# Kernel tuning notes

Measured on AMD Instinct MI355X. Metric: run time of the kernel, lower is better.

The kernel has to match this reference:

```python
import jax, jax.numpy as jnp
import numpy as np

B, L, D = 2, 4096, 1024      # batch, seq_len, d_model (expand_ratio=1 -> d_inner == D)
DS, RK, K = 16, 64, 3        # d_state, dt_rank, conv kernel size
EPS = 1e-5


def setup_inputs() -> dict:
    key = jax.random.key(0)
    ks = jax.random.split(key, 16)
    s = 0.02
    inp = {
        "x":      jax.random.normal(ks[0], (B, L, D), jnp.float32),
        "gamma":  jnp.ones((D,), jnp.float32),
        "beta":   jnp.zeros((D,), jnp.float32),
        "W_in":   jax.random.normal(ks[1], (D, 2 * D), jnp.float32) * s,
        "conv_w": jax.random.normal(ks[2], (K, 1, D), jnp.float32) * s,   # depthwise (k, 1, d)
        "conv_b": jnp.zeros((D,), jnp.float32),
        "W_xp":   jax.random.normal(ks[3], (D, RK), jnp.float32) * s,
        "W_Bg":   jax.random.normal(ks[4], (D, DS), jnp.float32) * s,
        "W_Cg":   jax.random.normal(ks[5], (D, DS), jnp.float32) * s,
        "W_dt":   jax.random.normal(ks[6], (RK, D), jnp.float32) * s,
        "b_dt":   jnp.zeros((D,), jnp.float32),
        "W_Bp":   jax.random.normal(ks[7], (DS, D), jnp.float32) * s,
        "W_Cp":   jax.random.normal(ks[8], (DS, D), jnp.float32) * s,
        "A":      -jnp.exp(jax.random.normal(ks[9], (D,), jnp.float32) * 0.5),  # negative for stability
        "D_skip": jnp.ones((D,), jnp.float32),
        "W_out":  jax.random.normal(ks[10], (D, D), jnp.float32) * s,
    }
    return inp


def reference(x, gamma, beta, W_in, conv_w, conv_b, W_xp, W_Bg, W_Cg,
              W_dt, b_dt, W_Bp, W_Cp, A, D_skip, W_out):
    d = x.shape[-1]
    # 1. LayerNorm
    mu = jnp.mean(x, -1, keepdims=True)
    var = jnp.mean(jnp.square(x - mu), -1, keepdims=True)
    xn = (x - mu) * jax.lax.rsqrt(var + EPS) * gamma + beta
    # 2. in_proj + split into main/gate branch
    xz = xn @ W_in                                 # (b, l, 2d)
    xb, z = jnp.split(xz, 2, axis=-1)
    # 3. depthwise Conv1D (same padding) + SiLU
    xc = jax.lax.conv_general_dilated(
        xb, conv_w, window_strides=(1,), padding='SAME',
        dimension_numbers=('NWC', 'WIO', 'NWC'), feature_group_count=d) + conv_b
    x_act = jax.nn.silu(xc)                        # (b, l, d)
    # SSM parameter generation
    delta = jax.nn.softplus((x_act @ W_xp) @ W_dt + b_dt)   # (b, l, d)
    Bm = (x_act @ W_Bg) @ W_Bp                     # (b, l, d)
    Cm = (x_act @ W_Cg) @ W_Cp                     # (b, l, d)
    # 4. diagonal selective scan: h_t = exp(delta*A)*h_{t-1} + delta*B*x ; y = C*h
    dA = jnp.exp(delta * A)
    dBx = delta * Bm * x_act
    def step(h, ab):
        a, bx = ab
        h = a * h + bx
        return h, h
    h0 = jnp.zeros_like(dA[:, 0])
    _, hs = jax.lax.scan(step, h0, (dA.transpose(1, 0, 2), dBx.transpose(1, 0, 2)))
    y = Cm * hs.transpose(1, 0, 2)
    # 5. skip-D, gating, out_proj + residual
    out_ssm = y + x_act * D_skip
    gated = out_ssm * jax.nn.silu(z)
    return gated @ W_out + x
```

## Files before the change

kernel.cpp:

```cpp
#include <hip/hip_runtime.h>
#include <math.h>

#define BB 2
#define LL 4096
#define DD 1024
#define DS 16
#define RK 64
#define MM (BB*LL)
#define NC 128
#define LC (LL/NC)

typedef __attribute__((ext_vector_type(8))) short short8;
typedef __attribute__((ext_vector_type(4))) float f32x4;

__device__ __forceinline__ unsigned short f2bf(float f) {
    union { float f; unsigned u; } v; v.f = f;
    unsigned r = v.u + 0x7fff + ((v.u >> 16) & 1);
    return (unsigned short)(r >> 16);
}
__device__ __forceinline__ float bf2f(unsigned short u) {
    union { unsigned u; float f; } v; v.u = ((unsigned)u) << 16;
    return v.f;
}
__device__ __forceinline__ float2 bf2x2(unsigned u) {
    return make_float2(bf2f((unsigned short)u), bf2f((unsigned short)(u >> 16)));
}
__device__ __forceinline__ unsigned f2bfx2(float lo, float hi) {
    return (unsigned)f2bf(lo) | ((unsigned)f2bf(hi) << 16);
}
__device__ __forceinline__ float fast_rcp(float x) {
    return __builtin_amdgcn_rcpf(x);
}
__device__ __forceinline__ float silu_f(float v) {
    return v * fast_rcp(1.0f + __expf(-v));
}
__device__ __forceinline__ void gload16(const void* g, void* l) {
    __builtin_amdgcn_global_load_lds(
        (const __attribute__((address_space(1))) unsigned int*)g,
        (__attribute__((address_space(3))) unsigned int*)l, 16, 0, 0);
}

__global__ __launch_bounds__(256)
void prep_misc(const float* __restrict__ W_in, const float* __restrict__ W_out,
               const float* __restrict__ W_xp, const float* __restrict__ W_Bg,
               const float* __restrict__ W_Cg, const float* __restrict__ W_dt,
               const float* __restrict__ W_Bp, const float* __restrict__ W_Cp,
               unsigned short* __restrict__ WinT, unsigned short* __restrict__ WoutT,
               unsigned short* __restrict__ WgT, unsigned short* __restrict__ WdtT,
               float* __restrict__ WBpT, float* __restrict__ WCpT,
               const float* __restrict__ x, const float* __restrict__ gamma,
               const float* __restrict__ beta, unsigned short* __restrict__ xn_bf) {
    __shared__ float t[32][33];
    __shared__ float ss[4], qq[4];
    int b = blockIdx.x;
    if (b >= 4224) {
        int row = b - 4224;
        int tid = threadIdx.x;
        const float4* xr = (const float4*)(x + (size_t)row * DD);
        float4 v = xr[tid];
        float s = v.x + v.y + v.z + v.w;
        float q = v.x*v.x + v.y*v.y + v.z*v.z + v.w*v.w;
        #pragma unroll
        for (int off = 32; off > 0; off >>= 1) {
            s += __shfl_down(s, off);
            q += __shfl_down(q, off);
        }
        int wv = tid >> 6;
        if ((tid & 63) == 0) { ss[wv] = s; qq[wv] = q; }
        __syncthreads();
        float S = ss[0] + ss[1] + ss[2] + ss[3];
        float Q = qq[0] + qq[1] + qq[2] + qq[3];
        float mu  = S * (1.0f / DD);
        float var = Q * (1.0f / DD) - mu * mu;
        float r = rsqrtf(var + 1e-5f);
        int d0 = tid * 4;
        float4 gv = *(const float4*)(gamma + d0);
        float4 bv = *(const float4*)(beta + d0);
        ushort4 o;
        o.x = f2bf((v.x - mu) * r * gv.x + bv.x);
        o.y = f2bf((v.y - mu) * r * gv.y + bv.y);
        o.z = f2bf((v.z - mu) * r * gv.z + bv.z);
        o.w = f2bf((v.w - mu) * r * gv.w + bv.w);
        *(ushort4*)&xn_bf[(size_t)row * DD + d0] = o;
    } else if (b < 3072) {
        const float* W; unsigned short* WT; int K, N, n0, k0;
        if (b < 2048) { W = W_in;  WT = WinT;  K = DD; N = 2 * DD;
                        n0 = (b & 63) * 32; k0 = (b >> 6) * 32; }
        else { int bb = b - 2048; W = W_out; WT = WoutT; K = DD; N = DD;
               n0 = (bb & 31) * 32; k0 = (bb >> 5) * 32; }
        int tx = threadIdx.x & 31, ty = threadIdx.x >> 5;
        #pragma unroll
        for (int r = 0; r < 32; r += 8)
            t[ty + r][tx] = W[(size_t)(k0 + ty + r) * N + n0 + tx];
        __syncthreads();
        #pragma unroll
        for (int r = 0; r < 32; r += 8) {
            int nl = ty + r;
            WT[(size_t)(n0 + nl) * K + k0 + tx] = f2bf(t[tx][nl]);
        }
    } else if (b < 3584) {
        int idx = (b - 3072) * 256 + threadIdx.x;
        int k = idx & 1023, n = idx >> 10;
        float v = 0.0f;
        if (n < 64)       v = W_xp[k * RK + n];
        else if (n < 80)  v = W_Bg[k * DS + (n - 64)];
        else if (n < 96)  v = W_Cg[k * DS + (n - 80)];
        WgT[idx] = f2bf(v);
    } else if (b < 4096) {
        int idx = (b - 3584) * 256 + threadIdx.x;
        int k = idx & 127, n = idx >> 7;
        float v = (k < 64) ? W_dt[k * 1024 + n] : 0.0f;
        WdtT[idx] = f2bf(v);
    } else if (b < 4160) {
        int idx = (b - 4096) * 256 + threadIdx.x;
        WBpT[idx] = W_Bp[(idx & 15) * 1024 + (idx >> 4)];
    } else {
        int idx = (b - 4160) * 256 + threadIdx.x;
        WCpT[idx] = W_Cp[(idx & 15) * 1024 + (idx >> 4)];
    }
}

#define MF(a, b, c) __builtin_amdgcn_mfma_f32_16x16x32_bf16(a, b, c, 0, 0, 0)
template<int EPI, int BM>
__global__ __launch_bounds__(512, 1)
void gemm256(const unsigned short* __restrict__ A, const unsigned short* __restrict__ BT,
             void* __restrict__ C0v, void* __restrict__ C1v,
             const float* __restrict__ res, int M, int N, int K) {
    constexpr int MR = BM / 32;
    constexpr int RA = BM / 64;
    constexpr int ABUF = BM * 64;
    extern __shared__ unsigned short sm[];
    unsigned short* As = sm;
    unsigned short* Bs = sm + 2 * ABUF;
    const int tid = threadIdx.x;
    const int wave = tid >> 6, lane = tid & 63;
    const int wr = wave >> 2, wc = wave & 3;
    const int fr = lane & 15, fs = lane >> 4;

    int nbx = gridDim.x;
    int nwg = nbx * gridDim.y;
    int bid = blockIdx.y * nbx + blockIdx.x;
    int cpx = nwg >> 3;
    int swz = (bid & 7) * cpx + (bid >> 3);
    int by = swz / nbx, bx = swz - by * nbx;
    size_t rb = (size_t)by * BM, cb = (size_t)bx * 256;

    const int srow = tid >> 3;
    const int ssw  = (tid & 7) ^ (srow & 7);
    const unsigned short* gA = A + (rb + srow) * K + ssw * 8;
    const unsigned short* gB = BT + (cb + srow) * K + ssw * 8;
    const size_t rstep = (size_t)64 * K;
    unsigned short* dA = As + tid * 8;
    unsigned short* dB = Bs + tid * 8;
    const int T = K >> 6;

#define STGA(rnd, buf, kt) gload16(gA + (size_t)(rnd) * rstep + (size_t)(kt) * 64, dA + (buf) * ABUF + (rnd) * 4096)
#define STGB(rnd, buf, kt) gload16(gB + (size_t)(rnd) * rstep + (size_t)(kt) * 64, dB + (buf) * 16384 + (rnd) * 4096)
#define FOFF(r, S) (((r) << 6) + ((((S) ^ ((r) & 7))) << 3))
#define LDA(i, kk) (*(const short8*)&Ab[FOFF(arow0 + ((i) << 4), fs + ((kk) << 2))])
#define LDB(j, kk) (*(const short8*)&Bb[FOFF(brow0 + ((j) << 4), fs + ((kk) << 2))])

    const int arow0 = wr * (BM / 2) + fr;
    const int brow0 = wc * 64 + fr;

    f32x4 acc[MR][4] = {};

    #pragma unroll
    for (int r = 0; r < RA; ++r) STGA(r, 0, 0);
    #pragma unroll
    for (int r = 0; r < 4; ++r) STGB(r, 0, 0);

    #pragma unroll 1
    for (int t = 0; t < T; ++t) {
        const int cur = t & 1, nx = cur ^ 1;
        const bool pf = (t + 1) < T;
        const unsigned short* Ab = As + cur * ABUF;
        const unsigned short* Bb = Bs + cur * 16384;

        if (pf) { STGA(0, nx, t + 1); STGB(0, nx, t + 1); }
        if (pf) { asm volatile("s_waitcnt vmcnt(2)" ::: "memory"); }
        else    { asm volatile("s_waitcnt vmcnt(0)" ::: "memory"); }
        __builtin_amdgcn_s_barrier();
        __builtin_amdgcn_sched_barrier(0);

        short8 bfr[4][2];
        #pragma unroll
        for (int j = 0; j < 4; ++j) {
            bfr[j][0] = LDB(j, 0);
            bfr[j][1] = LDB(j, 1);
        }
        __builtin_amdgcn_s_setprio(1);
        #pragma unroll
        for (int ii = 0; ii < MR / 4; ++ii) {
            short8 a0 = LDA(ii, 0), a1 = LDA(ii, 1);
            #pragma unroll
            for (int j = 0; j < 4; ++j) {
                acc[ii][j] = MF(a0, bfr[j][0], acc[ii][j]);
                acc[ii][j] = MF(a1, bfr[j][1], acc[ii][j]);
            }
        }
        __builtin_amdgcn_s_setprio(0);
        __builtin_amdgcn_sched_barrier(0);

        #pragma unroll
        for (int p = 1; p < 4; ++p) {
            if (pf) {
                if (p < RA) STGA(p, nx, t + 1);
                STGB(p, nx, t + 1);
            }
            __builtin_amdgcn_s_setprio(1);
            #pragma unroll
            for (int ii = 0; ii < MR / 4; ++ii) {
                const int i = p * (MR / 4) + ii;
                short8 a0 = LDA(i, 0), a1 = LDA(i, 1);
                #pragma unroll
                for (int j = 0; j < 4; ++j) {
                    acc[i][j] = MF(a0, bfr[j][0], acc[i][j]);
                    acc[i][j] = MF(a1, bfr[j][1], acc[i][j]);
                }
            }
            __builtin_amdgcn_s_setprio(0);
            __builtin_amdgcn_sched_barrier(0);
        }
        __builtin_amdgcn_s_barrier();
    }

    const int row0 = (int)rb + wr * (BM / 2) + fs * 4;
    const int col0 = (int)cb + wc * 64 + fr;
    if (EPI == 1) {
        unsigned short* Cd = (cb < DD) ? (unsigned short*)C0v : (unsigned short*)C1v;
        const int cadj = (cb < DD) ? 0 : -DD;
        #pragma unroll
        for (int i = 0; i < MR; ++i)
            #pragma unroll
            for (int j = 0; j < 4; ++j) {
                int col = col0 + cadj + (j << 4);
                #pragma unroll
                for (int q = 0; q < 4; ++q)
                    Cd[(size_t)(row0 + (i << 4) + q) * DD + col] = f2bf(acc[i][j][q]);
            }
    } else {
        float* C0 = (float*)C0v;
        #pragma unroll
        for (int i = 0; i < MR; ++i)
            #pragma unroll
            for (int j = 0; j < 4; ++j) {
                int col = col0 + (j << 4);
                #pragma unroll
                for (int q = 0; q < 4; ++q) {
                    size_t off = (size_t)(row0 + (i << 4) + q) * N + col;
                    C0[off] = acc[i][j][q] + res[off];
                }
            }
    }
#undef STGA
#undef STGB
#undef FOFF
#undef LDA
#undef LDB
}

__global__ __launch_bounds__(256)
void gemm_up(const unsigned short* __restrict__ A, const unsigned short* __restrict__ BT,
             unsigned short* __restrict__ C, const float* __restrict__ bias, int N) {
    __shared__ unsigned short As[128 * 128];
    __shared__ unsigned short Bs[128 * 128];
    int tid = threadIdx.x;
    int rb = blockIdx.y * 128, cb = blockIdx.x * 128;
    int wave = tid >> 6, lane = tid & 63;
    int wr = wave >> 1, wc = wave & 1;
    int fr = lane & 15, fs = lane >> 4;

    int srow16 = tid >> 4, sseg = tid & 15;
    #pragma unroll
    for (int r = 0; r < 8; ++r) {
        int row = r * 16 + srow16;
        int ss = sseg ^ (row & 15);
        gload16(A + (size_t)(rb + row) * 128 + ss * 8, (char*)As + r * 4096 + tid * 16);
        gload16(BT + (size_t)(cb + row) * 128 + ss * 8, (char*)Bs + r * 4096 + tid * 16);
    }
    asm volatile("s_waitcnt vmcnt(0)" ::: "memory");
    __syncthreads();

    f32x4 acc[4][4] = {};
    #pragma unroll
    for (int kk = 0; kk < 4; ++kk) {
        short8 af[4], bfr[4];
        #pragma unroll
        for (int i = 0; i < 4; ++i) {
            int row = (wr << 6) + (i << 4) + fr;
            int s = (fs + (kk << 2)) ^ (row & 15);
            af[i] = *(const short8*)&As[row * 128 + s * 8];
        }
        #pragma unroll
        for (int j = 0; j < 4; ++j) {
            int row = (wc << 6) + (j << 4) + fr;
            int s = (fs + (kk << 2)) ^ (row & 15);
            bfr[j] = *(const short8*)&Bs[row * 128 + s * 8];
        }
        #pragma unroll
        for (int i = 0; i < 4; ++i)
            #pragma unroll
            for (int j = 0; j < 4; ++j)
                acc[i][j] = MF(af[i], bfr[j], acc[i][j]);
    }

    int row0 = rb + (wr << 6) + (fs << 2);
    int col0 = (wc << 6) + fr;
    #pragma unroll
    for (int i = 0; i < 4; ++i)
        #pragma unroll
        for (int j = 0; j < 4; ++j) {
            int col = cb + col0 + (j << 4);
            float bv = bias[col];
            #pragma unroll
            for (int q = 0; q < 4; ++q) {
                float v = acc[i][j][q] + bv;
                v = fmaxf(v, 0.0f) + __logf(1.0f + __expf(-fabsf(v)));
                C[(size_t)(row0 + (i << 4) + q) * N + col] = f2bf(v);
            }
        }
}

__global__ __launch_bounds__(256)
void gemm_down(const unsigned short* __restrict__ A, const unsigned short* __restrict__ BT,
               unsigned short* __restrict__ C0, int M, int N, int K) {
    __shared__ unsigned short As[128 * 32];
    __shared__ unsigned short Bs[128 * 32];
    int tid = threadIdx.x;
    int rb = blockIdx.y * 128, cb = blockIdx.x * 128;
    int wave = tid >> 6, lane = tid & 63;
    int wr = wave >> 1, wc = wave & 1;
    int fr = lane & 15, fs = lane >> 4;

    int r0 = tid >> 2, s0 = tid & 3;
    int sw0 = s0 ^ ((r0 >> 1) & 3);
    const unsigned short* gA = A + (size_t)(rb + r0) * K + sw0 * 8;
    const unsigned short* gB = BT + (size_t)(cb + r0) * K + sw0 * 8;
    size_t half = (size_t)64 * K;
    char* lA0 = (char*)As + tid * 16;
    char* lA1 = (char*)As + (tid + 256) * 16;
    char* lB0 = (char*)Bs + tid * 16;
    char* lB1 = (char*)Bs + (tid + 256) * 16;

    int kb = blockIdx.z * (K >> 2), ke = kb + (K >> 2);

    f32x4 acc[4][4] = {};

    #pragma unroll 1
    for (int k0 = kb; k0 < ke; k0 += 32) {
        __syncthreads();
        gload16(gA + k0, lA0);
        gload16(gA + half + k0, lA1);
        gload16(gB + k0, lB0);
        gload16(gB + half + k0, lB1);
        __syncthreads();

        short8 af[4], bfr[4];
        #pragma unroll
        for (int i = 0; i < 4; i++) {
            int row = (wr << 6) + (i << 4) + fr;
            int off = (row << 5) + ((fs ^ ((row >> 1) & 3)) << 3);
            af[i] = *(const short8*)&As[off];
        }
        #pragma unroll
        for (int j = 0; j < 4; j++) {
            int row = (wc << 6) + (j << 4) + fr;
            int off = (row << 5) + ((fs ^ ((row >> 1) & 3)) << 3);
            bfr[j] = *(const short8*)&Bs[off];
        }
        #pragma unroll
        for (int i = 0; i < 4; i++)
            #pragma unroll
            for (int j = 0; j < 4; j++)
                acc[i][j] = MF(af[i], bfr[j], acc[i][j]);
    }

    int row0 = rb + (wr << 6) + (fs << 2);
    int col0 = (wc << 6) + fr;
    unsigned short* Cp = C0 + (size_t)blockIdx.z * M * N;
    #pragma unroll
    for (int i = 0; i < 4; i++)
        #pragma unroll
        for (int j = 0; j < 4; j++) {
            int col = cb + col0 + (j << 4);
            #pragma unroll
            for (int q = 0; q < 4; q++)
                Cp[(size_t)(row0 + (i << 4) + q) * N + col] = f2bf(acc[i][j][q]);
        }
}

__global__ __launch_bounds__(256)
void reduce_t(const unsigned short* __restrict__ tp, unsigned short* __restrict__ t_bf) {
    int idx = blockIdx.x * 256 + threadIdx.x;
    const size_t Q = (size_t)MM * 128;
    ushort4 a = ((const ushort4*)tp)[idx];
    ushort4 b = ((const ushort4*)(tp + Q))[idx];
    ushort4 c = ((const ushort4*)(tp + 2 * Q))[idx];
    ushort4 d = ((const ushort4*)(tp + 3 * Q))[idx];
    ushort4 o;
    o.x = f2bf(bf2f(a.x) + bf2f(b.x) + bf2f(c.x) + bf2f(d.x));
    o.y = f2bf(bf2f(a.y) + bf2f(b.y) + bf2f(c.y) + bf2f(d.y));
    o.z = f2bf(bf2f(a.z) + bf2f(b.z) + bf2f(c.z) + bf2f(d.z));
    o.w = f2bf(bf2f(a.w) + bf2f(b.w) + bf2f(c.w) + bf2f(d.w));
    ((ushort4*)t_bf)[idx] = o;
}

__global__ __launch_bounds__(256)
void conv_silu(const unsigned short* __restrict__ xb, const float* __restrict__ cw,
               const float* __restrict__ cb, unsigned short* __restrict__ xact) {
    int idx8 = blockIdx.x * 256 + threadIdx.x;
    size_t e = (size_t)idx8 * 8;
    int d0 = (int)(e & (DD - 1));
    int bl = (int)(e >> 10);
    int l = bl & (LL - 1);
    short8 cur = *(const short8*)&xb[e];
    short8 prv = {}, nxt = {};
    if (l > 0)      prv = *(const short8*)&xb[e - DD];
    if (l < LL - 1) nxt = *(const short8*)&xb[e + DD];
    short8 o;
    #pragma unroll
    for (int j = 0; j < 8; j++) {
        int d = d0 + j;
        float acc = cb[d];
        acc = fmaf(bf2f((unsigned short)prv[j]), cw[0 * DD + d], acc);
        acc = fmaf(bf2f((unsigned short)cur[j]), cw[1 * DD + d], acc);
        acc = fmaf(bf2f((unsigned short)nxt[j]), cw[2 * DD + d], acc);
        o[j] = (short)f2bf(silu_f(acc));
    }
    *(short8*)&xact[e] = o;
}

__global__ __launch_bounds__(256)
void scan_p1(const unsigned short* __restrict__ delta, const unsigned short* __restrict__ xact,
             const unsigned short* __restrict__ t_bf, const float* __restrict__ WBpT,
             const float* __restrict__ A, float* __restrict__ P, float* __restrict__ Hc) {
    __shared__ float tbs[LC][16];
    int tid = threadIdx.x;
    int d = (blockIdx.x * 256 + tid) * 2;
    int c = blockIdx.y, b = blockIdx.z;
    int row0 = b * LL + c * LC;
    {
        int rr = tid >> 3, kp = (tid & 7) * 2;
        float2 f = bf2x2(*(const unsigned*)&t_bf[(size_t)(row0 + rr) * 128 + 64 + kp]);
        tbs[rr][kp] = f.x; tbs[rr][kp + 1] = f.y;
    }
    __syncthreads();
    float wB0[16], wB1[16];
    #pragma unroll
    for (int j = 0; j < 4; ++j) {
        *(float4*)&wB0[j * 4] = *(const float4*)&WBpT[(size_t)d * 16 + j * 4];
        *(float4*)&wB1[j * 4] = *(const float4*)&WBpT[(size_t)(d + 1) * 16 + j * 4];
    }
    float2 a_d = *(const float2*)&A[d];
    float h0 = 0.0f, h1 = 0.0f, sd0 = 0.0f, sd1 = 0.0f;
    #pragma unroll 2
    for (int i = 0; i < LC; i++) {
        size_t o = (size_t)(row0 + i) * DD + d;
        float2 dl = bf2x2(*(const unsigned*)&delta[o]);
        float2 xa = bf2x2(*(const unsigned*)&xact[o]);
        float bm0 = 0.0f, bm1 = 0.0f;
        #pragma unroll
        for (int j = 0; j < 4; ++j) {
            float4 t4 = *(const float4*)&tbs[i][j * 4];
            bm0 = fmaf(t4.x, wB0[j*4+0], bm0); bm1 = fmaf(t4.x, wB1[j*4+0], bm1);
            bm0 = fmaf(t4.y, wB0[j*4+1], bm0); bm1 = fmaf(t4.y, wB1[j*4+1], bm1);
            bm0 = fmaf(t4.z, wB0[j*4+2], bm0); bm1 = fmaf(t4.z, wB1[j*4+2], bm1);
            bm0 = fmaf(t4.w, wB0[j*4+3], bm0); bm1 = fmaf(t4.w, wB1[j*4+3], bm1);
        }
        float a0 = __expf(dl.x * a_d.x);
        float a1 = __expf(dl.y * a_d.y);
        h0 = fmaf(a0, h0, dl.x * bm0 * xa.x);
        h1 = fmaf(a1, h1, dl.y * bm1 * xa.y);
        sd0 += dl.x; sd1 += dl.y;
    }
    int pc = (b * NC + c) * DD + d;
    *(float2*)&P[pc]  = make_float2(__expf(a_d.x * sd0), __expf(a_d.y * sd1));
    *(float2*)&Hc[pc] = make_float2(h0, h1);
}

__global__ __launch_bounds__(256)
void scan_p2(const float* __restrict__ P, const float* __restrict__ Hc,
             float* __restrict__ hin) {
    extern __shared__ float sP[];
    float* sH = sP + NC * 128;
    int b = blockIdx.y;
    int d0 = blockIdx.x * 128;
    for (int idx = threadIdx.x; idx < NC * 128; idx += 256) {
        int c = idx >> 7, dd = idx & 127;
        int o = (b * NC + c) * DD + d0 + dd;
        sP[idx] = P[o];
        sH[idx] = Hc[o];
    }
    __syncthreads();
    if (threadIdx.x < 128) {
        int dd = threadIdx.x;
        float carry = 0.0f;
        #pragma unroll 4
        for (int c = 0; c < NC; ++c) {
            float pv = sP[c * 128 + dd];
            float hv = sH[c * 128 + dd];
            sP[c * 128 + dd] = carry;
            carry = fmaf(pv, carry, hv);
        }
    }
    __syncthreads();
    for (int idx = threadIdx.x; idx < NC * 128; idx += 256) {
        int c = idx >> 7, dd = idx & 127;
        hin[(b * NC + c) * DD + d0 + dd] = sP[idx];
    }
}

__global__ __launch_bounds__(256)
void scan_p3(const unsigned short* __restrict__ delta, const unsigned short* __restrict__ xact,
             const unsigned short* __restrict__ zb, const unsigned short* __restrict__ t_bf,
             const float* __restrict__ WBpT, const float* __restrict__ WCpT,
             const float* __restrict__ hin, const float* __restrict__ A,
             const float* __restrict__ Dsk, unsigned short* __restrict__ g) {
    __shared__ float tbs[LC][16];
    __shared__ float tcs[LC][16];
    int tid = threadIdx.x;
    int d = (blockIdx.x * 256 + tid) * 2;
    int c = blockIdx.y, b = blockIdx.z;
    int row0 = b * LL + c * LC;
    {
        int rr = tid >> 3, kp = (tid & 7) * 2;
        const unsigned short* tr = &t_bf[(size_t)(row0 + rr) * 128];
        float2 fb = bf2x2(*(const unsigned*)&tr[64 + kp]);
        float2 fc = bf2x2(*(const unsigned*)&tr[80 + kp]);
        tbs[rr][kp] = fb.x; tbs[rr][kp + 1] = fb.y;
        tcs[rr][kp] = fc.x; tcs[rr][kp + 1] = fc.y;
    }
    __syncthreads();
    float wB0[16], wB1[16], wC0[16], wC1[16];
    #pragma unroll
    for (int j = 0; j < 4; ++j) {
        *(float4*)&wB0[j * 4] = *(const float4*)&WBpT[(size_t)d * 16 + j * 4];
        *(float4*)&wB1[j * 4] = *(const float4*)&WBpT[(size_t)(d + 1) * 16 + j * 4];
        *(float4*)&wC0[j * 4] = *(const float4*)&WCpT[(size_t)d * 16 + j * 4];
        *(float4*)&wC1[j * 4] = *(const float4*)&WCpT[(size_t)(d + 1) * 16 + j * 4];
    }
    float2 a_d = *(const float2*)&A[d];
    float2 dsk = *(const float2*)&Dsk[d];
    float2 hv = *(const float2*)&hin[(b * NC + c) * DD + d];
    float h0 = hv.x, h1 = hv.y;
    #pragma unroll 2
    for (int i = 0; i < LC; i++) {
        size_t o = (size_t)(row0 + i) * DD + d;
        float2 dl = bf2x2(*(const unsigned*)&delta[o]);
        float2 xa = bf2x2(*(const unsigned*)&xact[o]);
        float2 zv = bf2x2(*(const unsigned*)&zb[o]);
        float bm0 = 0.0f, bm1 = 0.0f, cm0 = 0.0f, cm1 = 0.0f;
        #pragma unroll
        for (int j = 0; j < 4; ++j) {
            float4 t4 = *(const float4*)&tbs[i][j * 4];
            float4 c4 = *(const float4*)&tcs[i][j * 4];
            bm0 = fmaf(t4.x, wB0[j*4+0], bm0); bm1 = fmaf(t4.x, wB1[j*4+0], bm1);
            bm0 = fmaf(t4.y, wB0[j*4+1], bm0); bm1 = fmaf(t4.y, wB1[j*4+1], bm1);
            bm0 = fmaf(t4.z, wB0[j*4+2], bm0); bm1 = fmaf(t4.z, wB1[j*4+2], bm1);
            bm0 = fmaf(t4.w, wB0[j*4+3], bm0); bm1 = fmaf(t4.w, wB1[j*4+3], bm1);
            cm0 = fmaf(c4.x, wC0[j*4+0], cm0); cm1 = fmaf(c4.x, wC1[j*4+0], cm1);
            cm0 = fmaf(c4.y, wC0[j*4+1], cm0); cm1 = fmaf(c4.y, wC1[j*4+1], cm1);
            cm0 = fmaf(c4.z, wC0[j*4+2], cm0); cm1 = fmaf(c4.z, wC1[j*4+2], cm1);
            cm0 = fmaf(c4.w, wC0[j*4+3], cm0); cm1 = fmaf(c4.w, wC1[j*4+3], cm1);
        }
        float a0 = __expf(dl.x * a_d.x);
        float a1 = __expf(dl.y * a_d.y);
        h0 = fmaf(a0, h0, dl.x * bm0 * xa.x);
        h1 = fmaf(a1, h1, dl.y * bm1 * xa.y);
        float os0 = fmaf(xa.x, dsk.x, cm0 * h0);
        float os1 = fmaf(xa.y, dsk.y, cm1 * h1);
        float g0 = os0 * silu_f(zv.x);
        float g1 = os1 * silu_f(zv.y);
        *(unsigned*)&g[o] = f2bfx2(g0, g1);
    }
}

extern "C" void kernel_launch(void* const* d_in, const int* in_sizes, int n_in,
                              void* d_out, int out_size, void* d_ws, size_t ws_size,
                              hipStream_t stream) {
    const float* x      = (const float*)d_in[0];
    const float* gamma  = (const float*)d_in[1];
    const float* beta   = (const float*)d_in[2];
    const float* W_in   = (const float*)d_in[3];
    const float* conv_w = (const float*)d_in[4];
    const float* conv_b = (const float*)d_in[5];
    const float* W_xp   = (const float*)d_in[6];
    const float* W_Bg   = (const float*)d_in[7];
    const float* W_Cg   = (const float*)d_in[8];
    const float* W_dt   = (const float*)d_in[9];
    const float* b_dt   = (const float*)d_in[10];
    const float* W_Bp   = (const float*)d_in[11];
    const float* W_Cp   = (const float*)d_in[12];
    const float* A      = (const float*)d_in[13];
    const float* Dsk    = (const float*)d_in[14];
    const float* W_out  = (const float*)d_in[15];
    float* out = (float*)d_out;

    const size_t BIG = (size_t)MM * DD;
    char* p = (char*)d_ws;
    unsigned short* xn_bf   = (unsigned short*)p;  p += BIG * 2;
    unsigned short* xb_bf   = (unsigned short*)p;  p += BIG * 2;
    unsigned short* z_bf    = (unsigned short*)p;  p += BIG * 2;
    unsigned short* xact_bf = (unsigned short*)p;  p += BIG * 2;
    unsigned short* delta_bf= (unsigned short*)p;  p += BIG * 2;
    unsigned short* t_bf    = (unsigned short*)p;  p += (size_t)MM * 128 * 2;
    unsigned short* tpart   = (unsigned short*)p;  p += (size_t)4 * MM * 128 * 2;
    float* P     = (float*)p;                      p += (size_t)BB * NC * DD * 4;
    float* Hc    = (float*)p;                      p += (size_t)BB * NC * DD * 4;
    float* hin   = (float*)p;                      p += (size_t)BB * NC * DD * 4;
    unsigned short* WinT  = (unsigned short*)p;    p += (size_t)2 * DD * DD * 2;
    unsigned short* WoutT = (unsigned short*)p;    p += (size_t)DD * DD * 2;
    unsigned short* WgT   = (unsigned short*)p;    p += (size_t)128 * DD * 2;
    unsigned short* WdtT  = (unsigned short*)p;    p += (size_t)DD * 128 * 2;
    float* WBpT = (float*)p;                       p += (size_t)DD * 16 * 4;
    float* WCpT = (float*)p;                       p += (size_t)DD * 16 * 4;
    unsigned short* g_bf  = xn_bf;

    {
        void (*k1)(const unsigned short*, const unsigned short*, void*, void*,
                   const float*, int, int, int) = gemm256<1, 256>;
        void (*k2)(const unsigned short*, const unsigned short*, void*, void*,
                   const float*, int, int, int) = gemm256<2, 128>;
        void (*k3)(const float*, const float*, float*) = scan_p2;
        (void)hipFuncSetAttribute((const void*)k1,
            hipFuncAttributeMaxDynamicSharedMemorySize, 131072);
        (void)hipFuncSetAttribute((const void*)k2,
            hipFuncAttributeMaxDynamicSharedMemorySize, 98304);
        (void)hipFuncSetAttribute((const void*)k3,
            hipFuncAttributeMaxDynamicSharedMemorySize, 131072);
    }

    prep_misc<<<4224 + MM, 256, 0, stream>>>(W_in, W_out, W_xp, W_Bg, W_Cg,
                                             W_dt, W_Bp, W_Cp,
                                             WinT, WoutT, WgT, WdtT, WBpT, WCpT,
                                             x, gamma, beta, xn_bf);
    gemm256<1, 256><<<dim3(2 * DD / 256, MM / 256), 512, 131072, stream>>>(
        xn_bf, WinT, xb_bf, z_bf, nullptr, MM, 2 * DD, DD);
    conv_silu<<<(MM * DD / 8) / 256, 256, 0, stream>>>(xb_bf, conv_w, conv_b, xact_bf);
    gemm_down<<<dim3(1, MM / 128, 4), 256, 0, stream>>>(
        xact_bf, WgT, tpart, MM, 128, DD);
    reduce_t<<<(MM * 128 / 4) / 256, 256, 0, stream>>>(tpart, t_bf);
    gemm_up<<<dim3(DD / 128, MM / 128), 256, 0, stream>>>(
        t_bf, WdtT, delta_bf, b_dt, DD);
    scan_p1<<<dim3(DD / 512, NC, BB), 256, 0, stream>>>(delta_bf, xact_bf, t_bf,
                                                        WBpT, A, P, Hc);
    scan_p2<<<dim3(DD / 128, BB), 256, 131072, stream>>>(P, Hc, hin);
    scan_p3<<<dim3(DD / 512, NC, BB), 256, 0, stream>>>(delta_bf, xact_bf, z_bf, t_bf,
                                                        WBpT, WCpT, hin, A, Dsk, g_bf);
    gemm256<2, 128><<<dim3(DD / 256, MM / 128), 512, 98304, stream>>>(
        g_bf, WoutT, out, nullptr, x, MM, DD, DD);
}
```

Measured before the change: 158.3 us.

## Process four channels per thread in scan kernels and double chunk count

Result: slower. 166.2 us (+5.0%).

```diff
diff --git a/kernel.cpp b/kernel.cpp
--- a/kernel.cpp
+++ b/kernel.cpp
@@ -7,7 +7,7 @@
 #define DS 16
 #define RK 64
 #define MM (BB*LL)
-#define NC 128
+#define NC 256
 #define LC (LL/NC)
 
 typedef __attribute__((ext_vector_type(8))) short short8;
@@ -21,9 +21,6 @@
 __device__ __forceinline__ float bf2f(unsigned short u) {
     union { unsigned u; float f; } v; v.u = ((unsigned)u) << 16;
     return v.f;
-}
-__device__ __forceinline__ float2 bf2x2(unsigned u) {
-    return make_float2(bf2f((unsigned short)u), bf2f((unsigned short)(u >> 16)));
 }
 __device__ __forceinline__ unsigned f2bfx2(float lo, float hi) {
     return (unsigned)f2bf(lo) | ((unsigned)f2bf(hi) << 16);
@@ -437,77 +434,87 @@
              const float* __restrict__ A, float* __restrict__ P, float* __restrict__ Hc) {
     __shared__ float tbs[LC][16];
     int tid = threadIdx.x;
-    int d = (blockIdx.x * 256 + tid) * 2;
+    int d = tid * 4;
     int c = blockIdx.y, b = blockIdx.z;
     int row0 = b * LL + c * LC;
     {
-        int rr = tid >> 3, kp = (tid & 7) * 2;
-        float2 f = bf2x2(*(const unsigned*)&t_bf[(size_t)(row0 + rr) * 128 + 64 + kp]);
-        tbs[rr][kp] = f.x; tbs[rr][kp + 1] = f.y;
+        int rr = tid >> 4, kp = tid & 15;
+        tbs[rr][kp] = bf2f(t_bf[(size_t)(row0 + rr) * 128 + 64 + kp]);
     }
     __syncthreads();
-    float wB0[16], wB1[16];
-    #pragma unroll
-    for (int j = 0; j < 4; ++j) {
-        *(float4*)&wB0[j * 4] = *(const float4*)&WBpT[(size_t)d * 16 + j * 4];
-        *(float4*)&wB1[j * 4] = *(const float4*)&WBpT[(size_t)(d + 1) * 16 + j * 4];
-    }
-    float2 a_d = *(const float2*)&A[d];
-    float h0 = 0.0f, h1 = 0.0f, sd0 = 0.0f, sd1 = 0.0f;
+    float wB[4][16];
+    #pragma unroll
+    for (int ch = 0; ch < 4; ++ch)
+        #pragma unroll
+        for (int j = 0; j < 4; ++j)
+            *(float4*)&wB[ch][j * 4] = *(const float4*)&WBpT[(size_t)(d + ch) * 16 + j * 4];
+    float4 a_d = *(const float4*)&A[d];
+    float ad[4] = {a_d.x, a_d.y, a_d.z, a_d.w};
+    float h[4] = {}, sd[4] = {};
     #pragma unroll 2
     for (int i = 0; i < LC; i++) {
         size_t o = (size_t)(row0 + i) * DD + d;
-        float2 dl = bf2x2(*(const unsigned*)&delta[o]);
-        float2 xa = bf2x2(*(const unsigned*)&xact[o]);
-        float bm0 = 0.0f, bm1 = 0.0f;
-        #pragma unroll
-        for (int j = 0; j < 4; ++j) {
-            float4 t4 = *(const float4*)&tbs[i][j * 4];
-            bm0 = fmaf(t4.x, wB0[j*4+0], bm0); bm1 = fmaf(t4.x, wB1[j*4+0], bm1);
-            bm0 = fmaf(t4.y, wB0[j*4+1], bm0); bm1 = fmaf(t4.y, wB1[j*4+1], bm1);
-            bm0 = fmaf(t4.z, wB0[j*4+2], bm0); bm1 = fmaf(t4.z, wB1[j*4+2], bm1);
-            bm0 = fmaf(t4.w, wB0[j*4+3], bm0); bm1 = fmaf(t4.w, wB1[j*4+3], bm1);
-        }
-        float a0 = __expf(dl.x * a_d.x);
-        float a1 = __expf(dl.y * a_d.y);
-        h0 = fmaf(a0, h0, dl.x * bm0 * xa.x);
-        h1 = fmaf(a1, h1, dl.y * bm1 * xa.y);
-        sd0 += dl.x; sd1 += dl.y;
+        ushort4 dlu = *(const ushort4*)&delta[o];
+        ushort4 xau = *(const ushort4*)&xact[o];
+        unsigned short dla[4] = {dlu.x, dlu.y, dlu.z, dlu.w};
+        unsigned short xaa[4] = {xau.x, xau.y, xau.z, xau.w};
+        float trow[16];
+        #pragma unroll
+        for (int j = 0; j < 4; ++j)
+            *(float4*)&trow[j * 4] = *(const float4*)&tbs[i][j * 4];
+        #pragma unroll
+        for (int ch = 0; ch < 4; ++ch) {
+            float dl = bf2f(dla[ch]);
+            float xa = bf2f(xaa[ch]);
+            float bm = 0.0f;
+            #pragma unroll
+            for (int k = 0; k < 16; ++k)
+                bm = fmaf(trow[k], wB[ch][k], bm);
+            float a = __expf(dl * ad[ch]);
+            h[ch] = fmaf(a, h[ch], dl * bm * xa);
+            sd[ch] += dl;
+        }
     }
     int pc = (b * NC + c) * DD + d;
-    *(float2*)&P[pc]  = make_float2(__expf(a_d.x * sd0), __expf(a_d.y * sd1));
-    *(float2*)&Hc[pc] = make_float2(h0, h1);
+    *(float4*)&P[pc] = make_float4(__expf(ad[0] * sd[0]), __expf(ad[1] * sd[1]),
+                                   __expf(ad[2] * sd[2]), __expf(ad[3] * sd[3]));
+    *(float4*)&Hc[pc] = make_float4(h[0], h[1], h[2], h[3]);
 }
 
 __global__ __launch_bounds__(256)
 void scan_p2(const float* __restrict__ P, const float* __restrict__ Hc,
              float* __restrict__ hin) {
     extern __shared__ float sP[];
-    float* sH = sP + NC * 128;
+    float* sH = sP + 128 * 128;
     int b = blockIdx.y;
     int d0 = blockIdx.x * 128;
-    for (int idx = threadIdx.x; idx < NC * 128; idx += 256) {
-        int c = idx >> 7, dd = idx & 127;
-        int o = (b * NC + c) * DD + d0 + dd;
-        sP[idx] = P[o];
-        sH[idx] = Hc[o];
-    }
-    __syncthreads();
-    if (threadIdx.x < 128) {
-        int dd = threadIdx.x;
-        float carry = 0.0f;
-        #pragma unroll 4
-        for (int c = 0; c < NC; ++c) {
-            float pv = sP[c * 128 + dd];
-            float hv = sH[c * 128 + dd];
-            sP[c * 128 + dd] = carry;
-            carry = fmaf(pv, carry, hv);
-        }
-    }
-    __syncthreads();
-    for (int idx = threadIdx.x; idx < NC * 128; idx += 256) {
-        int c = idx >> 7, dd = idx & 127;
-        hin[(b * NC + c) * DD + d0 + dd] = sP[idx];
+    int dd = threadIdx.x;
+    float carry = 0.0f;
+    #pragma unroll 1
+    for (int pass = 0; pass < NC / 128; ++pass) {
+        int cbase = pass * 128;
+        for (int idx = threadIdx.x; idx < 128 * 128; idx += 256) {
+            int c = idx >> 7, dl = idx & 127;
+            int o = (b * NC + cbase + c) * DD + d0 + dl;
+            sP[idx] = P[o];
+            sH[idx] = Hc[o];
+        }
+        __syncthreads();
+        if (dd < 128) {
+            #pragma unroll 4
+            for (int c = 0; c < 128; ++c) {
+                float pv = sP[c * 128 + dd];
+                float hv = sH[c * 128 + dd];
+                sP[c * 128 + dd] = carry;
+                carry = fmaf(pv, carry, hv);
+            }
+        }
+        __syncthreads();
+        for (int idx = threadIdx.x; idx < 128 * 128; idx += 256) {
+            int c = idx >> 7, dl = idx & 127;
+            hin[(b * NC + cbase + c) * DD + d0 + dl] = sP[idx];
+        }
+        __syncthreads();
     }
 }
 
@@ -520,59 +527,66 @@
     __shared__ float tbs[LC][16];
     __shared__ float tcs[LC][16];
     int tid = threadIdx.x;
-    int d = (blockIdx.x * 256 + tid) * 2;
+    int d = tid * 4;
     int c = blockIdx.y, b = blockIdx.z;
     int row0 = b * LL + c * LC;
     {
-        int rr = tid >> 3, kp = (tid & 7) * 2;
+        int rr = tid >> 4, kp = tid & 15;
         const unsigned short* tr = &t_bf[(size_t)(row0 + rr) * 128];
-        float2 fb = bf2x2(*(const unsigned*)&tr[64 + kp]);
-        float2 fc = bf2x2(*(const unsigned*)&tr[80 + kp]);
-        tbs[rr][kp] = fb.x; tbs[rr][kp + 1] = fb.y;
-        tcs[rr][kp] = fc.x; tcs[rr][kp + 1] = fc.y;
+        tbs[rr][kp] = bf2f(tr[64 + kp]);
+        tcs[rr][kp] = bf2f(tr[80 + kp]);
     }
     __syncthreads();
-    float wB0[16], wB1[16], wC0[16], wC1[16];
-    #pragma unroll
-    for (int j = 0; j < 4; ++j) {
-        *(float4*)&wB0[j * 4] = *(const float4*)&WBpT[(size_t)d * 16 + j * 4];
-        *(float4*)&wB1[j * 4] = *(const float4*)&WBpT[(size_t)(d + 1) * 16 + j * 4];
-        *(float4*)&wC0[j * 4] = *(const float4*)&WCpT[(size_t)d * 16 + j * 4];
-        *(float4*)&wC1[j * 4] = *(const float4*)&WCpT[(size_t)(d + 1) * 16 + j * 4];
-    }
-    float2 a_d = *(const float2*)&A[d];
-    float2 dsk = *(const float2*)&Dsk[d];
-    float2 hv = *(const float2*)&hin[(b * NC + c) * DD + d];
-    float h0 = hv.x, h1 = hv.y;
+    float wB[4][16], wC[4][16];
+    #pragma unroll
+    for (int ch = 0; ch < 4; ++ch)
+        #pragma unroll
+        for (int j = 0; j < 4; ++j) {
+            *(float4*)&wB[ch][j * 4] = *(const float4*)&WBpT[(size_t)(d + ch) * 16 + j * 4];
+            *(float4*)&wC[ch][j * 4] = *(const float4*)&WCpT[(size_t)(d + ch) * 16 + j * 4];
+        }
+    float4 a_d = *(const float4*)&A[d];
+    float4 dskv = *(const float4*)&Dsk[d];
+    float ad[4] = {a_d.x, a_d.y, a_d.z, a_d.w};
+    float dsk[4] = {dskv.x, dskv.y, dskv.z, dskv.w};
+    float4 hv = *(const float4*)&hin[(b * NC + c) * DD + d];
+    float h[4] = {hv.x, hv.y, hv.z, hv.w};
     #pragma unroll 2
     for (int i = 0; i < LC; i++) {
         size_t o = (size_t)(row0 + i) * DD + d;
-        float2 dl = bf2x2(*(const unsigned*)&delta[o]);
-        float2 xa = bf2x2(*(const unsigned*)&xact[o]);
-        float2 zv = bf2x2(*(const unsigned*)&zb[o]);
-        float bm0 = 0.0f, bm1 = 0.0f, cm0 = 0.0f, cm1 = 0.0f;
+        ushort4 dlu = *(const ushort4*)&delta[o];
+        ushort4 xau = *(const ushort4*)&xact[o];
+        ushort4 zvu = *(const ushort4*)&zb[o];
+        unsigned short dla[4] = {dlu.x, dlu.y, dlu.z, dlu.w};
+        unsigned short xaa[4] = {xau.x, xau.y, xau.z, xau.w};
+        unsigned short zva[4] = {zvu.x, zvu.y, zvu.z, zvu.w};
+        float trow[16], crow[16];
         #pragma unroll
         for (int j = 0; j < 4; ++j) {
-            float4 t4 = *(const float4*)&tbs[i][j * 4];
-            float4 c4 = *(const float4*)&tcs[i][j * 4];
-            bm0 = fmaf(t4.x, wB0[j*4+0], bm0); bm1 = fmaf(t4.x, wB1[j*4+0], bm1);
-            bm0 = fmaf(t4.y, wB0[j*4+1], bm0); bm1 = fmaf(t4.y, wB1[j*4+1], bm1);
-            bm0 = fmaf(t4.z, wB0[j*4+2], bm0); bm1 = fmaf(t4.z, wB1[j*4+2], bm1);
-            bm0 = fmaf(t4.w, wB0[j*4+3], bm0); bm1 = fmaf(t4.w, wB1[j*4+3], bm1);
-            cm0 = fmaf(c4.x, wC0[j*4+0], cm0); cm1 = fmaf(c4.x, wC1[j*4+0], cm1);
-            cm0 = fmaf(c4.y, wC0[j*4+1], cm0); cm1 = fmaf(c4.y, wC1[j*4+1], cm1);
-            cm0 = fmaf(c4.z, wC0[j*4+2], cm0); cm1 = fmaf(c4.z, wC1[j*4+2], cm1);
-            cm0 = fmaf(c4.w, wC0[j*4+3], cm0); cm1 = fmaf(c4.w, wC1[j*4+3], cm1);
-        }
-        float a0 = __expf(dl.x * a_d.x);
-        float a1 = __expf(dl.y * a_d.y);
-        h0 = fmaf(a0, h0, dl.x * bm0 * xa.x);
-        h1 = fmaf(a1, h1, dl.y * bm1 * xa.y);
-        float os0 = fmaf(xa.x, dsk.x, cm0 * h0);
-        float os1 = fmaf(xa.y, dsk.y, cm1 * h1);
-        float g0 = os0 * silu_f(zv.x);
-        float g1 = os1 * silu_f(zv.y);
-        *(unsigned*)&g[o] = f2bfx2(g0, g1);
+            *(float4*)&trow[j * 4] = *(const float4*)&tbs[i][j * 4];
+            *(float4*)&crow[j * 4] = *(const float4*)&tcs[i][j * 4];
+        }
+        float gv[4];
+        #pragma unroll
+        for (int ch = 0; ch < 4; ++ch) {
+            float dl = bf2f(dla[ch]);
+            float xa = bf2f(xaa[ch]);
+            float zv = bf2f(zva[ch]);
+            float bm = 0.0f, cm = 0.0f;
+            #pragma unroll
+            for (int k = 0; k < 16; ++k) {
+                bm = fmaf(trow[k], wB[ch][k], bm);
+                cm = fmaf(crow[k], wC[ch][k], cm);
+            }
+            float a = __expf(dl * ad[ch]);
+            h[ch] = fmaf(a, h[ch], dl * bm * xa);
+            float os = fmaf(xa, dsk[ch], cm * h[ch]);
+            gv[ch] = os * silu_f(zv);
+        }
+        uint2 pk;
+        pk.x = f2bfx2(gv[0], gv[1]);
+        pk.y = f2bfx2(gv[2], gv[3]);
+        *(uint2*)&g[o] = pk;
     }
 }
 
@@ -643,11 +657,11 @@
     reduce_t<<<(MM * 128 / 4) / 256, 256, 0, stream>>>(tpart, t_bf);
     gemm_up<<<dim3(DD / 128, MM / 128), 256, 0, stream>>>(
         t_bf, WdtT, delta_bf, b_dt, DD);
-    scan_p1<<<dim3(DD / 512, NC, BB), 256, 0, stream>>>(delta_bf, xact_bf, t_bf,
-                                                        WBpT, A, P, Hc);
+    scan_p1<<<dim3(1, NC, BB), 256, 0, stream>>>(delta_bf, xact_bf, t_bf,
+                                                 WBpT, A, P, Hc);
     scan_p2<<<dim3(DD / 128, BB), 256, 131072, stream>>>(P, Hc, hin);
-    scan_p3<<<dim3(DD / 512, NC, BB), 256, 0, stream>>>(delta_bf, xact_bf, z_bf, t_bf,
-                                                        WBpT, WCpT, hin, A, Dsk, g_bf);
+    scan_p3<<<dim3(1, NC, BB), 256, 0, stream>>>(delta_bf, xact_bf, z_bf, t_bf,
+                                                 WBpT, WCpT, hin, A, Dsk, g_bf);
     gemm256<2, 128><<<dim3(DD / 256, MM / 128), 512, 98304, stream>>>(
         g_bf, WoutT, out, nullptr, x, MM, DD, DD);
 }
```
